# Kernel optimization log

Hardware: AMD Instinct MI355X
Metric: run time of the kernel (lower is better)

## Reference

```python
import jax, jax.numpy as jnp
import numpy as np

CONF_THRESH = 0.3
NMS_THRESH = 0.5
TOP_K = 64
VAR = (0.1, 0.2)  # standard SSD decode variances


def setup_inputs() -> dict:
    key = jax.random.key(0)
    k1, k2, k3 = jax.random.split(key, 3)
    B, A, C = 16, 16384, 81
    loc = jax.random.normal(k1, (B, A, 4), jnp.float32)
    conf = jax.random.normal(k2, (B, A, C), jnp.float32)
    anchors = jax.random.uniform(k3, (A, 4), jnp.float32)  # cxcywh in [0,1]
    return {"loc": loc, "conf": conf, "anchors": anchors}


def _decode(loc, anchors):
    # SSD-style decode: loc [A,4] offsets, anchors [A,4] cxcywh -> corners [A,4]
    cxcy = anchors[:, :2] + loc[:, :2] * VAR[0] * anchors[:, 2:]
    wh = anchors[:, 2:] * jnp.exp(loc[:, 2:] * VAR[1])
    tl = cxcy - wh * 0.5
    return jnp.concatenate([tl, tl + wh], axis=1)


def _iou(box, boxes):
    # box [4], boxes [A,4] in corner format
    tl = jnp.maximum(box[:2], boxes[:, :2])
    br = jnp.minimum(box[2:], boxes[:, 2:])
    wh = jnp.clip(br - tl, 0.0)
    inter = wh[:, 0] * wh[:, 1]
    a1 = (box[2] - box[0]) * (box[3] - box[1])
    a2 = (boxes[:, 2] - boxes[:, 0]) * (boxes[:, 3] - boxes[:, 1])
    return inter / (a1 + a2 - inter)


def _nms(boxes, scores):
    # greedy NMS for one (batch, class) lane; boxes [A,4], scores [A]
    s0 = jnp.where(scores > CONF_THRESH, scores, -1.0)

    def step(s, _):
        i = jnp.argmax(s)
        sc = s[i]
        box = boxes[i]
        keep = sc > 0.0  # -1 means masked/suppressed; valid scores > conf_thresh > 0
        supp = jnp.where(_iou(box, boxes) > NMS_THRESH, -1.0, s).at[i].set(-1.0)
        s_next = jnp.where(keep, supp, s)
        row = jnp.where(keep, jnp.concatenate([sc[None], box]),
                        jnp.zeros((5,), s.dtype))
        return s_next, row

    _, rows = jax.lax.scan(step, s0, None, length=TOP_K)
    return rows  # [TOP_K, 5] = (score, x1, y1, x2, y2), zero-padded


def reference(loc, conf, anchors):
    conf = jax.nn.sigmoid(conf)                      # [B,A,C]
    boxes = jax.vmap(_decode, in_axes=(0, None))(loc, anchors)  # [B,A,4]
    scores = jnp.swapaxes(conf, 1, 2)                # [B,C,A]
    per_class = jax.vmap(_nms, in_axes=(None, 0))    # over classes
    out = jax.vmap(per_class)(boxes, scores)         # [B,C,TOP_K,5]
    return out
```

## Files before the change

### kernel.cpp

```cpp
#include <hip/hip_runtime.h>
#include <math.h>

constexpr int B_N  = 16;
constexpr int A_N  = 16384;
constexpr int C_N  = 81;
constexpr int TOPK = 64;
constexpr int DNT  = 256;
constexpr int NBINS = 232;
constexpr int CAP   = 512;
constexpr unsigned BIN_BASE = 0x3E99u;

constexpr int TA   = 64;
constexpr int TPAD = 85;
constexpr int TNT  = 256;
constexpr int TILE_ELEMS = TA * C_N;
constexpr int TILE_F4    = (TA / 4) * C_N;

constexpr int SNT = 256;

__global__ __launch_bounds__(DNT) void decode_kernel(const float4* __restrict__ loc,
                                                     const float4* __restrict__ anch,
                                                     float4* __restrict__ boxes) {
    int i = blockIdx.x * DNT + threadIdx.x;
    int a = i & (A_N - 1);
    float4 l  = loc[i];
    float4 an = anch[a];
    float cx = an.x + (l.x * 0.1f) * an.z;
    float cy = an.y + (l.y * 0.1f) * an.w;
    float w  = an.z * expf(l.z * 0.2f);
    float h  = an.w * expf(l.w * 0.2f);
    float x1 = cx - w * 0.5f;
    float y1 = cy - h * 0.5f;
    boxes[i] = make_float4(x1, y1, x1 + w, y1 + h);
}

__global__ __launch_bounds__(TNT) void sigT_kernel(const float* __restrict__ conf,
                                                   float* __restrict__ scoresT) {
    __shared__ float tile[TA][TPAD];

    const int a0 = blockIdx.x * TA;
    const int b  = blockIdx.y;
    const int t  = threadIdx.x;

    const float* src = conf + ((size_t)b * A_N + a0) * C_N;
#pragma unroll
    for (int i = 0; i < (TILE_ELEMS + TNT - 1) / TNT; ++i) {
        int idx = i * TNT + t;
        if (idx < TILE_ELEMS) {
            float x  = src[idx];
            int   al = idx / C_N;
            int   cc = idx - al * C_N;
            tile[al][cc] = 1.0f / (1.0f + expf(-x));
        }
    }
    __syncthreads();
    float* dst = scoresT + (size_t)b * C_N * A_N + a0;
#pragma unroll
    for (int i = 0; i < (TILE_F4 + TNT - 1) / TNT; ++i) {
        int idx4 = i * TNT + t;
        if (idx4 < TILE_F4) {
            int cc  = idx4 >> 4;
            int al4 = idx4 & 15;
            float4 v;
            v.x = tile[al4 * 4 + 0][cc];
            v.y = tile[al4 * 4 + 1][cc];
            v.z = tile[al4 * 4 + 2][cc];
            v.w = tile[al4 * 4 + 3][cc];
            ((float4*)(dst + (size_t)cc * A_N))[al4] = v;
        }
    }
}

__global__ __launch_bounds__(SNT, 4) void select_nms_kernel(
        const float* __restrict__ scoresT,
        const float4* __restrict__ boxes,
        float* __restrict__ out) {
    __shared__ int hist[NBINS];
    __shared__ unsigned long long cand[CAP];
    __shared__ float4 cbox[CAP];
    __shared__ int s_cnt, s_acc, s_kout;

    const int bc   = blockIdx.x;
    const int b    = bc / C_N;
    const int t    = threadIdx.x;
    const int lane = t & 63;
    const int wv   = t >> 6;

    for (int i = t; i < NBINS; i += SNT) hist[i] = 0;
    if (t == 0) { s_acc = 0; s_kout = 0; }
    __syncthreads();

    const float4* sptr = (const float4*)(scoresT + (size_t)bc * A_N);
    const float4* bptr = boxes + (size_t)b * A_N;
    float* optr = out + (size_t)bc * TOPK * 5;

    for (int i = 0; i < A_N / 4 / SNT; ++i) {
        float4 s4 = sptr[t + SNT * i];
        float s[4] = {s4.x, s4.y, s4.z, s4.w};
#pragma unroll
        for (int q = 0; q < 4; ++q) {
            if (s[q] > 0.3f) {
                unsigned u = __float_as_uint(s[q]);
                int bin = (int)(u >> 16) - (int)BIN_BASE;
                bin = bin < 0 ? 0 : (bin > NBINS - 1 ? NBINS - 1 : bin);
                atomicAdd(&hist[bin], 1);
            }
        }
    }
    __syncthreads();

    float rx1 = 0.f, ry1 = 0.f, rx2 = 0.f, ry2 = 0.f, rar = 0.f;
    int acc = 0, kout = 0;

    int bin_hi = NBINS;
    for (;;) {
        int lo = bin_hi, tot = 0;
        while (lo > 0) {
            int cnt = hist[lo - 1];
            if (tot + cnt > CAP) {
                if (tot == 0) { lo--; }
                break;
            }
            tot += cnt; lo--;
        }
        const int bin_lo = lo;
        if (bin_lo == bin_hi) break;
        if (t == 0) s_cnt = 0;
        __syncthreads();

        for (int i = 0; i < A_N / 4 / SNT; ++i) {
            float4 s4 = sptr[t + SNT * i];
            float s[4] = {s4.x, s4.y, s4.z, s4.w};
#pragma unroll
            for (int q = 0; q < 4; ++q) {
                if (s[q] > 0.3f) {
                    unsigned u = __float_as_uint(s[q]);
                    int bin = (int)(u >> 16) - (int)BIN_BASE;
                    bin = bin < 0 ? 0 : (bin > NBINS - 1 ? NBINS - 1 : bin);
                    if (bin >= bin_lo && bin < bin_hi) {
                        int slot = atomicAdd(&s_cnt, 1);
                        if (slot < CAP) {
                            unsigned a = (unsigned)(4 * (t + SNT * i) + q);
                            cand[slot] = ((unsigned long long)u << 32) | (unsigned)(~a);
                        }
                    }
                }
            }
        }
        __syncthreads();
        int C = s_cnt; if (C > CAP) C = CAP;

        if (C > 0) {
            if (wv == 0) {
                unsigned long long key[8];
#pragma unroll
                for (int r = 0; r < 8; ++r) {
                    int sidx = r * 64 + lane;
                    key[r] = (sidx < C) ? cand[sidx] : 0ull;
                }
#pragma unroll
                for (int k = 2; k <= CAP; k <<= 1) {
#pragma unroll
                    for (int j = k >> 1; j > 0; j >>= 1) {
                        if (j >= 64) {
                            int jr = j >> 6;
#pragma unroll
                            for (int r = 0; r < 8; ++r) {
                                int rp = r ^ jr;
                                if (rp > r) {
                                    int e = r * 64 + lane;
                                    bool up = ((e & k) == 0);
                                    unsigned long long va = key[r], vb = key[rp];
                                    bool sw = up ? (va < vb) : (va > vb);
                                    if (sw) { key[r] = vb; key[rp] = va; }
                                }
                            }
                        } else {
#pragma unroll
                            for (int r = 0; r < 8; ++r) {
                                int e = r * 64 + lane;
                                bool up    = ((e & k) == 0);
                                bool isLow = ((lane & j) == 0);
                                unsigned long long va = key[r];
                                unsigned long long vb = __shfl_xor(va, j, 64);
                                bool keepMax = (up == isLow);
                                key[r] = keepMax ? (va > vb ? va : vb)
                                                 : (va < vb ? va : vb);
                            }
                        }
                    }
                }
#pragma unroll
                for (int r = 0; r < 8; ++r) cand[r * 64 + lane] = key[r];
            }
            __syncthreads();

            for (int e = t; e < CAP; e += SNT)
                if (e < C) cbox[e] = bptr[(int)(~(unsigned)cand[e])];
            __syncthreads();

            if (wv == 0) {
                int ts = 0;
                unsigned long long k0 = cand[0];
                float4 cb = cbox[0];
                while (ts < C) {
                    unsigned long long nk = 0ull;
                    float4 nb = cb;
                    if (ts + 1 < C) { nk = cand[ts + 1]; nb = cbox[ts + 1]; }
                    float sc = __uint_as_float((unsigned)(k0 >> 32));
                    float ca = (cb.z - cb.x) * (cb.w - cb.y);
                    bool over = false;
                    if (lane < acc) {
                        float tlx = fmaxf(rx1, cb.x);
                        float tly = fmaxf(ry1, cb.y);
                        float brx = fminf(rx2, cb.z);
                        float bry = fminf(ry2, cb.w);
                        float iw  = fmaxf(brx - tlx, 0.0f);
                        float ih  = fmaxf(bry - tly, 0.0f);
                        float inter = iw * ih;
                        float iou = inter / (rar + ca - inter);
                        over = iou > 0.5f;
                    }
                    if (!__any(over)) {
                        if (lane == acc) { rx1 = cb.x; ry1 = cb.y; rx2 = cb.z; ry2 = cb.w; rar = ca; }
                        if (lane == 0) {
                            float* o = optr + (size_t)kout * 5;
                            o[0] = sc; o[1] = cb.x; o[2] = cb.y; o[3] = cb.z; o[4] = cb.w;
                        }
                        acc++; kout++;
                        if (acc == TOPK) break;
                    }
                    ++ts; k0 = nk; cb = nb;
                }
                if (lane == 0) { s_acc = acc; s_kout = kout; }
            }
            __syncthreads();
            if (s_acc >= TOPK) break;
        }
        bin_hi = bin_lo;
    }

    {
        const int ko = s_kout;
        float* o  = optr + (size_t)ko * 5;
        int   rem = (TOPK - ko) * 5;
        for (int i = t; i < rem; i += SNT) o[i] = 0.0f;
    }
}

__device__ __forceinline__ void sort_gather_scan64(
        unsigned long long* cand, float4* cbox, int C, int lane,
        const float4* __restrict__ bptr, float* __restrict__ optr,
        float& rx1, float& ry1, float& rx2, float& ry2, float& rar,
        int& acc, int& kout) {
    unsigned long long key[8];
#pragma unroll
    for (int r = 0; r < 8; ++r) {
        int sidx = r * 64 + lane;
        key[r] = (sidx < C) ? cand[sidx] : 0ull;
    }
#pragma unroll
    for (int k = 2; k <= CAP; k <<= 1) {
#pragma unroll
        for (int j = k >> 1; j > 0; j >>= 1) {
            if (j >= 64) {
                int jr = j >> 6;
#pragma unroll
                for (int r = 0; r < 8; ++r) {
                    int rp = r ^ jr;
                    if (rp > r) {
                        int e = r * 64 + lane;
                        bool up = ((e & k) == 0);
                        unsigned long long va = key[r], vb = key[rp];
                        bool sw = up ? (va < vb) : (va > vb);
                        if (sw) { key[r] = vb; key[rp] = va; }
                    }
                }
            } else {
#pragma unroll
                for (int r = 0; r < 8; ++r) {
                    int e = r * 64 + lane;
                    bool up    = ((e & k) == 0);
                    bool isLow = ((lane & j) == 0);
                    unsigned long long va = key[r];
                    unsigned long long vb = __shfl_xor(va, j, 64);
                    bool keepMax = (up == isLow);
                    key[r] = keepMax ? (va > vb ? va : vb) : (va < vb ? va : vb);
                }
            }
        }
    }
    __syncthreads();
#pragma unroll
    for (int r = 0; r < 8; ++r) cand[r * 64 + lane] = key[r];
    __syncthreads();
#pragma unroll
    for (int r = 0; r < 8; ++r) {
        int e = r * 64 + lane;
        if (e < C) cbox[e] = bptr[(int)(~(unsigned)cand[e])];
    }
    __syncthreads();

    int t = 0;
    unsigned long long k0 = cand[0];
    float4 cb = cbox[0];
    while (t < C) {
        unsigned long long nk = 0ull;
        float4 nb = cb;
        if (t + 1 < C) { nk = cand[t + 1]; nb = cbox[t + 1]; }
        float sc = __uint_as_float((unsigned)(k0 >> 32));
        float ca = (cb.z - cb.x) * (cb.w - cb.y);
        bool over = false;
        if (lane < acc) {
            float tlx = fmaxf(rx1, cb.x);
            float tly = fmaxf(ry1, cb.y);
            float brx = fminf(rx2, cb.z);
            float bry = fminf(ry2, cb.w);
            float iw  = fmaxf(brx - tlx, 0.0f);
            float ih  = fmaxf(bry - tly, 0.0f);
            float inter = iw * ih;
            float iou = inter / (rar + ca - inter);
            over = iou > 0.5f;
        }
        if (!__any(over)) {
            if (lane == acc) { rx1 = cb.x; ry1 = cb.y; rx2 = cb.z; ry2 = cb.w; rar = ca; }
            if (lane == 0) {
                float* o = optr + (size_t)kout * 5;
                o[0] = sc; o[1] = cb.x; o[2] = cb.y; o[3] = cb.z; o[4] = cb.w;
            }
            acc++; kout++;
            if (acc == TOPK) break;
        }
        ++t; k0 = nk; cb = nb;
    }
}

__global__ __launch_bounds__(64, 4) void nms_fallback(const float* __restrict__ conf,
                                                      const float4* __restrict__ boxes,
                                                      float* __restrict__ out) {
    __shared__ int hist[NBINS];
    __shared__ unsigned long long cand[CAP];
    __shared__ float4 cbox[CAP];
    __shared__ int s_cnt;

    const int c    = blockIdx.x;
    const int b    = blockIdx.y;
    const int lane = threadIdx.x;

    const float4* bptr = boxes + (size_t)b * A_N;
    const float*  cptr = conf + (size_t)b * A_N * C_N + c;
    float* optr = out + (size_t)(b * C_N + c) * TOPK * 5;

    for (int i = lane; i < NBINS; i += 64) hist[i] = 0;
    __syncthreads();
    for (int i = 0; i < A_N / 256; ++i) {
        int a0 = 4 * (lane + 64 * i);
#pragma unroll
        for (int q = 0; q < 4; ++q) {
            float x = cptr[(size_t)(a0 + q) * C_N];
            float s = 1.0f / (1.0f + expf(-x));
            if (s > 0.3f) {
                unsigned u = __float_as_uint(s);
                int bin = (int)(u >> 16) - (int)BIN_BASE;
                bin = bin < 0 ? 0 : (bin > NBINS - 1 ? NBINS - 1 : bin);
                atomicAdd(&hist[bin], 1);
            }
        }
    }
    __syncthreads();

    float rx1 = 0.f, ry1 = 0.f, rx2 = 0.f, ry2 = 0.f, rar = 0.f;
    int acc = 0, kout = 0;
    int bin_hi = NBINS;
    for (;;) {
        int lo = bin_hi, tot = 0;
        while (lo > 0) {
            int cnt = hist[lo - 1];
            if (tot + cnt > CAP) { if (tot == 0) { lo--; } break; }
            tot += cnt; lo--;
        }
        const int bin_lo = lo;
        if (bin_lo == bin_hi) break;
        if (lane == 0) s_cnt = 0;
        __syncthreads();
        for (int i = 0; i < A_N / 256; ++i) {
            int a0 = 4 * (lane + 64 * i);
#pragma unroll
            for (int q = 0; q < 4; ++q) {
                float x = cptr[(size_t)(a0 + q) * C_N];
                float s = 1.0f / (1.0f + expf(-x));
                if (s > 0.3f) {
                    unsigned u = __float_as_uint(s);
                    int bin = (int)(u >> 16) - (int)BIN_BASE;
                    bin = bin < 0 ? 0 : (bin > NBINS - 1 ? NBINS - 1 : bin);
                    if (bin >= bin_lo && bin < bin_hi) {
                        int slot = atomicAdd(&s_cnt, 1);
                        if (slot < CAP)
                            cand[slot] = ((unsigned long long)u << 32) | (unsigned)(~(unsigned)(a0 + q));
                    }
                }
            }
        }
        __syncthreads();
        int C = s_cnt; if (C > CAP) C = CAP;
        if (C > 0)
            sort_gather_scan64(cand, cbox, C, lane, bptr, optr,
                               rx1, ry1, rx2, ry2, rar, acc, kout);
        if (acc == TOPK) break;
        bin_hi = bin_lo;
    }
    {
        float* o  = optr + (size_t)kout * 5;
        int   rem = (TOPK - kout) * 5;
        for (int i = lane; i < rem; i += 64) o[i] = 0.0f;
    }
}

extern "C" void kernel_launch(void* const* d_in, const int* in_sizes, int n_in,
                              void* d_out, int out_size, void* d_ws, size_t ws_size,
                              hipStream_t stream) {
    const float* loc     = (const float*)d_in[0];
    const float* conf    = (const float*)d_in[1];
    const float* anchors = (const float*)d_in[2];
    float* out = (float*)d_out;

    const size_t boxes_bytes  = (size_t)B_N * A_N * sizeof(float4);
    const size_t scores_bytes = (size_t)B_N * C_N * A_N * sizeof(float);

    float4* boxes = (float4*)d_ws;

    decode_kernel<<<(B_N * A_N) / DNT, DNT, 0, stream>>>(
        (const float4*)loc, (const float4*)anchors, boxes);

    if (ws_size >= boxes_bytes + scores_bytes) {
        float* scoresT = (float*)((char*)d_ws + boxes_bytes);
        sigT_kernel<<<dim3(A_N / TA, B_N), TNT, 0, stream>>>(conf, scoresT);
        select_nms_kernel<<<dim3(B_N * C_N), SNT, 0, stream>>>(scoresT, boxes, out);
    } else {
        nms_fallback<<<dim3(C_N, B_N), 64, 0, stream>>>(conf, boxes, out);
    }
}
```

Measured before the change: 220.6 us.

## Use single-wave select-NMS blocks and vectorized float4 sigmoid loads in transpose

The select/NMS kernel now runs with one 64-thread wave per (batch,class) instead of 256 threads, reusing the existing wave-level sort/gather/scan helper. This removes the block-wide barriers and the idle waves during the sort and scan phases, but each wave now scans all 16384 scores by itself. The sigmoid-transpose kernel also loads conf as float4 into an unpadded flat shared tile, where the old version used scalar loads. This may add shared-memory bank conflicts on the strided transposed reads.

```diff
diff --git a/kernel.cpp b/kernel.cpp
--- a/kernel.cpp
+++ b/kernel.cpp
@@ -11,12 +11,9 @@
 constexpr unsigned BIN_BASE = 0x3E99u;
 
 constexpr int TA   = 64;
-constexpr int TPAD = 85;
 constexpr int TNT  = 256;
 constexpr int TILE_ELEMS = TA * C_N;
-constexpr int TILE_F4    = (TA / 4) * C_N;
-
-constexpr int SNT = 256;
+constexpr int TILE_F4    = TILE_ELEMS / 4;
 
 __global__ __launch_bounds__(DNT) void decode_kernel(const float4* __restrict__ loc,
                                                      const float4* __restrict__ anch,
@@ -36,21 +33,25 @@
 
 __global__ __launch_bounds__(TNT) void sigT_kernel(const float* __restrict__ conf,
                                                    float* __restrict__ scoresT) {
-    __shared__ float tile[TA][TPAD];
+    __shared__ float4 tile4[TILE_F4];
+    float* tile = (float*)tile4;
 
     const int a0 = blockIdx.x * TA;
     const int b  = blockIdx.y;
     const int t  = threadIdx.x;
 
-    const float* src = conf + ((size_t)b * A_N + a0) * C_N;
-#pragma unroll
-    for (int i = 0; i < (TILE_ELEMS + TNT - 1) / TNT; ++i) {
-        int idx = i * TNT + t;
-        if (idx < TILE_ELEMS) {
-            float x  = src[idx];
-            int   al = idx / C_N;
-            int   cc = idx - al * C_N;
-            tile[al][cc] = 1.0f / (1.0f + expf(-x));
+    const float4* src = (const float4*)(conf + ((size_t)b * A_N + a0) * C_N);
+#pragma unroll
+    for (int i = 0; i < (TILE_F4 + TNT - 1) / TNT; ++i) {
+        int idx4 = i * TNT + t;
+        if (idx4 < TILE_F4) {
+            float4 x = src[idx4];
+            float4 v;
+            v.x = 1.0f / (1.0f + expf(-x.x));
+            v.y = 1.0f / (1.0f + expf(-x.y));
+            v.z = 1.0f / (1.0f + expf(-x.z));
+            v.w = 1.0f / (1.0f + expf(-x.w));
+            tile4[idx4] = v;
         }
     }
     __syncthreads();
@@ -61,190 +62,14 @@
         if (idx4 < TILE_F4) {
             int cc  = idx4 >> 4;
             int al4 = idx4 & 15;
+            int e   = al4 * 4 * C_N + cc;
             float4 v;
-            v.x = tile[al4 * 4 + 0][cc];
-            v.y = tile[al4 * 4 + 1][cc];
-            v.z = tile[al4 * 4 + 2][cc];
-            v.w = tile[al4 * 4 + 3][cc];
+            v.x = tile[e];
+            v.y = tile[e + C_N];
+            v.z = tile[e + 2 * C_N];
+            v.w = tile[e + 3 * C_N];
             ((float4*)(dst + (size_t)cc * A_N))[al4] = v;
         }
-    }
-}
-
-__global__ __launch_bounds__(SNT, 4) void select_nms_kernel(
-        const float* __restrict__ scoresT,
-        const float4* __restrict__ boxes,
-        float* __restrict__ out) {
-    __shared__ int hist[NBINS];
-    __shared__ unsigned long long cand[CAP];
-    __shared__ float4 cbox[CAP];
-    __shared__ int s_cnt, s_acc, s_kout;
-
-    const int bc   = blockIdx.x;
-    const int b    = bc / C_N;
-    const int t    = threadIdx.x;
-    const int lane = t & 63;
-    const int wv   = t >> 6;
-
-    for (int i = t; i < NBINS; i += SNT) hist[i] = 0;
-    if (t == 0) { s_acc = 0; s_kout = 0; }
-    __syncthreads();
-
-    const float4* sptr = (const float4*)(scoresT + (size_t)bc * A_N);
-    const float4* bptr = boxes + (size_t)b * A_N;
-    float* optr = out + (size_t)bc * TOPK * 5;
-
-    for (int i = 0; i < A_N / 4 / SNT; ++i) {
-        float4 s4 = sptr[t + SNT * i];
-        float s[4] = {s4.x, s4.y, s4.z, s4.w};
-#pragma unroll
-        for (int q = 0; q < 4; ++q) {
-            if (s[q] > 0.3f) {
-                unsigned u = __float_as_uint(s[q]);
-                int bin = (int)(u >> 16) - (int)BIN_BASE;
-                bin = bin < 0 ? 0 : (bin > NBINS - 1 ? NBINS - 1 : bin);
-                atomicAdd(&hist[bin], 1);
-            }
-        }
-    }
-    __syncthreads();
-
-    float rx1 = 0.f, ry1 = 0.f, rx2 = 0.f, ry2 = 0.f, rar = 0.f;
-    int acc = 0, kout = 0;
-
-    int bin_hi = NBINS;
-    for (;;) {
-        int lo = bin_hi, tot = 0;
-        while (lo > 0) {
-            int cnt = hist[lo - 1];
-            if (tot + cnt > CAP) {
-                if (tot == 0) { lo--; }
-                break;
-            }
-            tot += cnt; lo--;
-        }
-        const int bin_lo = lo;
-        if (bin_lo == bin_hi) break;
-        if (t == 0) s_cnt = 0;
-        __syncthreads();
-
-        for (int i = 0; i < A_N / 4 / SNT; ++i) {
-            float4 s4 = sptr[t + SNT * i];
-            float s[4] = {s4.x, s4.y, s4.z, s4.w};
-#pragma unroll
-            for (int q = 0; q < 4; ++q) {
-                if (s[q] > 0.3f) {
-                    unsigned u = __float_as_uint(s[q]);
-                    int bin = (int)(u >> 16) - (int)BIN_BASE;
-                    bin = bin < 0 ? 0 : (bin > NBINS - 1 ? NBINS - 1 : bin);
-                    if (bin >= bin_lo && bin < bin_hi) {
-                        int slot = atomicAdd(&s_cnt, 1);
-                        if (slot < CAP) {
-                            unsigned a = (unsigned)(4 * (t + SNT * i) + q);
-                            cand[slot] = ((unsigned long long)u << 32) | (unsigned)(~a);
-                        }
-                    }
-                }
-            }
-        }
-        __syncthreads();
-        int C = s_cnt; if (C > CAP) C = CAP;
-
-        if (C > 0) {
-            if (wv == 0) {
-                unsigned long long key[8];
-#pragma unroll
-                for (int r = 0; r < 8; ++r) {
-                    int sidx = r * 64 + lane;
-                    key[r] = (sidx < C) ? cand[sidx] : 0ull;
-                }
-#pragma unroll
-                for (int k = 2; k <= CAP; k <<= 1) {
-#pragma unroll
-                    for (int j = k >> 1; j > 0; j >>= 1) {
-                        if (j >= 64) {
-                            int jr = j >> 6;
-#pragma unroll
-                            for (int r = 0; r < 8; ++r) {
-                                int rp = r ^ jr;
-                                if (rp > r) {
-                                    int e = r * 64 + lane;
-                                    bool up = ((e & k) == 0);
-                                    unsigned long long va = key[r], vb = key[rp];
-                                    bool sw = up ? (va < vb) : (va > vb);
-                                    if (sw) { key[r] = vb; key[rp] = va; }
-                                }
-                            }
-                        } else {
-#pragma unroll
-                            for (int r = 0; r < 8; ++r) {
-                                int e = r * 64 + lane;
-                                bool up    = ((e & k) == 0);
-                                bool isLow = ((lane & j) == 0);
-                                unsigned long long va = key[r];
-                                unsigned long long vb = __shfl_xor(va, j, 64);
-                                bool keepMax = (up == isLow);
-                                key[r] = keepMax ? (va > vb ? va : vb)
-                                                 : (va < vb ? va : vb);
-                            }
-                        }
-                    }
-                }
-#pragma unroll
-                for (int r = 0; r < 8; ++r) cand[r * 64 + lane] = key[r];
-            }
-            __syncthreads();
-
-            for (int e = t; e < CAP; e += SNT)
-                if (e < C) cbox[e] = bptr[(int)(~(unsigned)cand[e])];
-            __syncthreads();
-
-            if (wv == 0) {
-                int ts = 0;
-                unsigned long long k0 = cand[0];
-                float4 cb = cbox[0];
-                while (ts < C) {
-                    unsigned long long nk = 0ull;
-                    float4 nb = cb;
-                    if (ts + 1 < C) { nk = cand[ts + 1]; nb = cbox[ts + 1]; }
-                    float sc = __uint_as_float((unsigned)(k0 >> 32));
-                    float ca = (cb.z - cb.x) * (cb.w - cb.y);
-                    bool over = false;
-                    if (lane < acc) {
-                        float tlx = fmaxf(rx1, cb.x);
-                        float tly = fmaxf(ry1, cb.y);
-                        float brx = fminf(rx2, cb.z);
-                        float bry = fminf(ry2, cb.w);
-                        float iw  = fmaxf(brx - tlx, 0.0f);
-                        float ih  = fmaxf(bry - tly, 0.0f);
-                        float inter = iw * ih;
-                        float iou = inter / (rar + ca - inter);
-                        over = iou > 0.5f;
-                    }
-                    if (!__any(over)) {
-                        if (lane == acc) { rx1 = cb.x; ry1 = cb.y; rx2 = cb.z; ry2 = cb.w; rar = ca; }
-                        if (lane == 0) {
-                            float* o = optr + (size_t)kout * 5;
-                            o[0] = sc; o[1] = cb.x; o[2] = cb.y; o[3] = cb.z; o[4] = cb.w;
-                        }
-                        acc++; kout++;
-                        if (acc == TOPK) break;
-                    }
-                    ++ts; k0 = nk; cb = nb;
-                }
-                if (lane == 0) { s_acc = acc; s_kout = kout; }
-            }
-            __syncthreads();
-            if (s_acc >= TOPK) break;
-        }
-        bin_hi = bin_lo;
-    }
-
-    {
-        const int ko = s_kout;
-        float* o  = optr + (size_t)ko * 5;
-        int   rem = (TOPK - ko) * 5;
-        for (int i = t; i < rem; i += SNT) o[i] = 0.0f;
     }
 }
 
@@ -301,13 +126,13 @@
     }
     __syncthreads();
 
-    int t = 0;
+    int ts = 0;
     unsigned long long k0 = cand[0];
     float4 cb = cbox[0];
-    while (t < C) {
+    while (ts < C) {
         unsigned long long nk = 0ull;
         float4 nb = cb;
-        if (t + 1 < C) { nk = cand[t + 1]; nb = cbox[t + 1]; }
+        if (ts + 1 < C) { nk = cand[ts + 1]; nb = cbox[ts + 1]; }
         float sc = __uint_as_float((unsigned)(k0 >> 32));
         float ca = (cb.z - cb.x) * (cb.w - cb.y);
         bool over = false;
@@ -331,7 +156,99 @@
             acc++; kout++;
             if (acc == TOPK) break;
         }
-        ++t; k0 = nk; cb = nb;
+        ++ts; k0 = nk; cb = nb;
+    }
+}
+
+__global__ __launch_bounds__(64, 4) void select_nms_kernel(
+        const float* __restrict__ scoresT,
+        const float4* __restrict__ boxes,
+        float* __restrict__ out) {
+    __shared__ int hist[NBINS];
+    __shared__ unsigned long long cand[CAP];
+    __shared__ float4 cbox[CAP];
+    __shared__ int s_cnt;
+
+    const int bc   = blockIdx.x;
+    const int b    = bc / C_N;
+    const int lane = threadIdx.x;
+
+    for (int i = lane; i < NBINS; i += 64) hist[i] = 0;
+    __syncthreads();
+
+    const float4* sptr = (const float4*)(scoresT + (size_t)bc * A_N);
+    const float4* bptr = boxes + (size_t)b * A_N;
+    float* optr = out + (size_t)bc * TOPK * 5;
+
+#pragma unroll 8
+    for (int i = 0; i < A_N / 4 / 64; ++i) {
+        float4 s4 = sptr[lane + 64 * i];
+        float s[4] = {s4.x, s4.y, s4.z, s4.w};
+#pragma unroll
+        for (int q = 0; q < 4; ++q) {
+            if (s[q] > 0.3f) {
+                unsigned u = __float_as_uint(s[q]);
+                int bin = (int)(u >> 16) - (int)BIN_BASE;
+                bin = bin < 0 ? 0 : (bin > NBINS - 1 ? NBINS - 1 : bin);
+                atomicAdd(&hist[bin], 1);
+            }
+        }
+    }
+    __syncthreads();
+
+    float rx1 = 0.f, ry1 = 0.f, rx2 = 0.f, ry2 = 0.f, rar = 0.f;
+    int acc = 0, kout = 0;
+
+    int bin_hi = NBINS;
+    for (;;) {
+        int lo = bin_hi, tot = 0;
+        while (lo > 0) {
+            int cnt = hist[lo - 1];
+            if (tot + cnt > CAP) {
+                if (tot == 0) { lo--; }
+                break;
+            }
+            tot += cnt; lo--;
+        }
+        const int bin_lo = lo;
+        if (bin_lo == bin_hi) break;
+        if (lane == 0) s_cnt = 0;
+        __syncthreads();
+
+#pragma unroll 8
+        for (int i = 0; i < A_N / 4 / 64; ++i) {
+            float4 s4 = sptr[lane + 64 * i];
+            float s[4] = {s4.x, s4.y, s4.z, s4.w};
+#pragma unroll
+            for (int q = 0; q < 4; ++q) {
+                if (s[q] > 0.3f) {
+                    unsigned u = __float_as_uint(s[q]);
+                    int bin = (int)(u >> 16) - (int)BIN_BASE;
+                    bin = bin < 0 ? 0 : (bin > NBINS - 1 ? NBINS - 1 : bin);
+                    if (bin >= bin_lo && bin < bin_hi) {
+                        int slot = atomicAdd(&s_cnt, 1);
+                        if (slot < CAP) {
+                            unsigned a = (unsigned)(4 * (lane + 64 * i) + q);
+                            cand[slot] = ((unsigned long long)u << 32) | (unsigned)(~a);
+                        }
+                    }
+                }
+            }
+        }
+        __syncthreads();
+        int C = s_cnt; if (C > CAP) C = CAP;
+
+        if (C > 0)
+            sort_gather_scan64(cand, cbox, C, lane, bptr, optr,
+                               rx1, ry1, rx2, ry2, rar, acc, kout);
+        if (acc == TOPK) break;
+        bin_hi = bin_lo;
+    }
+
+    {
+        float* o  = optr + (size_t)kout * 5;
+        int   rem = (TOPK - kout) * 5;
+        for (int i = lane; i < rem; i += 64) o[i] = 0.0f;
     }
 }
 
@@ -435,7 +352,7 @@
     if (ws_size >= boxes_bytes + scores_bytes) {
         float* scoresT = (float*)((char*)d_ws + boxes_bytes);
         sigT_kernel<<<dim3(A_N / TA, B_N), TNT, 0, stream>>>(conf, scoresT);
-        select_nms_kernel<<<dim3(B_N * C_N), SNT, 0, stream>>>(scoresT, boxes, out);
+        select_nms_kernel<<<dim3(B_N * C_N), 64, 0, stream>>>(scoresT, boxes, out);
     } else {
         nms_fallback<<<dim3(C_N, B_N), 64, 0, stream>>>(conf, boxes, out);
     }
```

New measurement: 258.7 us. +17.3%, slower.

## Split select+NMS into histogram/candidate kernel and single-wave sorted NMS kernel

Applied to the files above, without the earlier changes.

The fused select+NMS kernel is split in two. A 256-thread select kernel builds the score histogram and writes the top-bin candidates to global workspace. A separate 64-thread NMS kernel then sorts those candidates and runs the serial greedy scan, rescanning scores only when it needs more candidates. Separately, the sigmoid/transpose kernel now loads conf with float4 vectorized reads into an unpadded shared tile. The split stops the serial NMS phase from idling three waves per block, at the cost of an extra launch, global round trips for candidates and histograms, and possible LDS bank conflicts from removing the padding.

```diff
diff --git a/kernel.cpp b/kernel.cpp
--- a/kernel.cpp
+++ b/kernel.cpp
@@ -9,14 +9,13 @@
 constexpr int NBINS = 232;
 constexpr int CAP   = 512;
 constexpr unsigned BIN_BASE = 0x3E99u;
+constexpr int SNT = 256;
+constexpr int BC_N = B_N * C_N;
 
 constexpr int TA   = 64;
-constexpr int TPAD = 85;
 constexpr int TNT  = 256;
 constexpr int TILE_ELEMS = TA * C_N;
-constexpr int TILE_F4    = (TA / 4) * C_N;
-
-constexpr int SNT = 256;
+constexpr int TILE_F4    = TILE_ELEMS / 4;
 
 __global__ __launch_bounds__(DNT) void decode_kernel(const float4* __restrict__ loc,
                                                      const float4* __restrict__ anch,
@@ -36,21 +35,25 @@
 
 __global__ __launch_bounds__(TNT) void sigT_kernel(const float* __restrict__ conf,
                                                    float* __restrict__ scoresT) {
-    __shared__ float tile[TA][TPAD];
+    __shared__ float4 tile4[TILE_F4];
+    float* tile = (float*)tile4;
 
     const int a0 = blockIdx.x * TA;
     const int b  = blockIdx.y;
     const int t  = threadIdx.x;
 
-    const float* src = conf + ((size_t)b * A_N + a0) * C_N;
-#pragma unroll
-    for (int i = 0; i < (TILE_ELEMS + TNT - 1) / TNT; ++i) {
-        int idx = i * TNT + t;
-        if (idx < TILE_ELEMS) {
-            float x  = src[idx];
-            int   al = idx / C_N;
-            int   cc = idx - al * C_N;
-            tile[al][cc] = 1.0f / (1.0f + expf(-x));
+    const float4* src = (const float4*)(conf + ((size_t)b * A_N + a0) * C_N);
+#pragma unroll
+    for (int i = 0; i < (TILE_F4 + TNT - 1) / TNT; ++i) {
+        int idx4 = i * TNT + t;
+        if (idx4 < TILE_F4) {
+            float4 x = src[idx4];
+            float4 v;
+            v.x = 1.0f / (1.0f + expf(-x.x));
+            v.y = 1.0f / (1.0f + expf(-x.y));
+            v.z = 1.0f / (1.0f + expf(-x.z));
+            v.w = 1.0f / (1.0f + expf(-x.w));
+            tile4[idx4] = v;
         }
     }
     __syncthreads();
@@ -61,17 +64,264 @@
         if (idx4 < TILE_F4) {
             int cc  = idx4 >> 4;
             int al4 = idx4 & 15;
+            int e   = al4 * 4 * C_N + cc;
             float4 v;
-            v.x = tile[al4 * 4 + 0][cc];
-            v.y = tile[al4 * 4 + 1][cc];
-            v.z = tile[al4 * 4 + 2][cc];
-            v.w = tile[al4 * 4 + 3][cc];
+            v.x = tile[e];
+            v.y = tile[e + C_N];
+            v.z = tile[e + 2 * C_N];
+            v.w = tile[e + 3 * C_N];
             ((float4*)(dst + (size_t)cc * A_N))[al4] = v;
         }
     }
 }
 
-__global__ __launch_bounds__(SNT, 4) void select_nms_kernel(
+__device__ __forceinline__ void sort_gather_scan64(
+        unsigned long long* cand, float4* cbox, int C, int lane,
+        const float4* __restrict__ bptr, float* __restrict__ optr,
+        float& rx1, float& ry1, float& rx2, float& ry2, float& rar,
+        int& acc, int& kout) {
+    unsigned long long key[8];
+#pragma unroll
+    for (int r = 0; r < 8; ++r) {
+        int sidx = r * 64 + lane;
+        key[r] = (sidx < C) ? cand[sidx] : 0ull;
+    }
+#pragma unroll
+    for (int k = 2; k <= CAP; k <<= 1) {
+#pragma unroll
+        for (int j = k >> 1; j > 0; j >>= 1) {
+            if (j >= 64) {
+                int jr = j >> 6;
+#pragma unroll
+                for (int r = 0; r < 8; ++r) {
+                    int rp = r ^ jr;
+                    if (rp > r) {
+                        int e = r * 64 + lane;
+                        bool up = ((e & k) == 0);
+                        unsigned long long va = key[r], vb = key[rp];
+                        bool sw = up ? (va < vb) : (va > vb);
+                        if (sw) { key[r] = vb; key[rp] = va; }
+                    }
+                }
+            } else {
+#pragma unroll
+                for (int r = 0; r < 8; ++r) {
+                    int e = r * 64 + lane;
+                    bool up    = ((e & k) == 0);
+                    bool isLow = ((lane & j) == 0);
+                    unsigned long long va = key[r];
+                    unsigned long long vb = __shfl_xor(va, j, 64);
+                    bool keepMax = (up == isLow);
+                    key[r] = keepMax ? (va > vb ? va : vb) : (va < vb ? va : vb);
+                }
+            }
+        }
+    }
+    __syncthreads();
+#pragma unroll
+    for (int r = 0; r < 8; ++r) cand[r * 64 + lane] = key[r];
+    __syncthreads();
+#pragma unroll
+    for (int r = 0; r < 8; ++r) {
+        int e = r * 64 + lane;
+        if (e < C) cbox[e] = bptr[(int)(~(unsigned)cand[e])];
+    }
+    __syncthreads();
+
+    int ts = 0;
+    unsigned long long k0 = cand[0];
+    float4 cb = cbox[0];
+    while (ts < C) {
+        unsigned long long nk = 0ull;
+        float4 nb = cb;
+        if (ts + 1 < C) { nk = cand[ts + 1]; nb = cbox[ts + 1]; }
+        float sc = __uint_as_float((unsigned)(k0 >> 32));
+        float ca = (cb.z - cb.x) * (cb.w - cb.y);
+        bool over = false;
+        if (lane < acc) {
+            float tlx = fmaxf(rx1, cb.x);
+            float tly = fmaxf(ry1, cb.y);
+            float brx = fminf(rx2, cb.z);
+            float bry = fminf(ry2, cb.w);
+            float iw  = fmaxf(brx - tlx, 0.0f);
+            float ih  = fmaxf(bry - tly, 0.0f);
+            float inter = iw * ih;
+            float iou = inter / (rar + ca - inter);
+            over = iou > 0.5f;
+        }
+        if (!__any(over)) {
+            if (lane == acc) { rx1 = cb.x; ry1 = cb.y; rx2 = cb.z; ry2 = cb.w; rar = ca; }
+            if (lane == 0) {
+                float* o = optr + (size_t)kout * 5;
+                o[0] = sc; o[1] = cb.x; o[2] = cb.y; o[3] = cb.z; o[4] = cb.w;
+            }
+            acc++; kout++;
+            if (acc == TOPK) break;
+        }
+        ++ts; k0 = nk; cb = nb;
+    }
+}
+
+__global__ __launch_bounds__(SNT) void select_kernel(
+        const float* __restrict__ scoresT,
+        unsigned long long* __restrict__ g_cand,
+        int* __restrict__ g_hist,
+        int* __restrict__ g_cnt,
+        int* __restrict__ g_blo) {
+    __shared__ int hist[NBINS];
+    __shared__ int s_cnt;
+
+    const int bc = blockIdx.x;
+    const int t  = threadIdx.x;
+
+    for (int i = t; i < NBINS; i += SNT) hist[i] = 0;
+    if (t == 0) s_cnt = 0;
+    __syncthreads();
+
+    const float4* sptr = (const float4*)(scoresT + (size_t)bc * A_N);
+
+    for (int i = 0; i < A_N / 4 / SNT; ++i) {
+        float4 s4 = sptr[t + SNT * i];
+        float s[4] = {s4.x, s4.y, s4.z, s4.w};
+#pragma unroll
+        for (int q = 0; q < 4; ++q) {
+            if (s[q] > 0.3f) {
+                unsigned u = __float_as_uint(s[q]);
+                int bin = (int)(u >> 16) - (int)BIN_BASE;
+                bin = bin < 0 ? 0 : (bin > NBINS - 1 ? NBINS - 1 : bin);
+                atomicAdd(&hist[bin], 1);
+            }
+        }
+    }
+    __syncthreads();
+
+    for (int i = t; i < NBINS; i += SNT) g_hist[bc * NBINS + i] = hist[i];
+
+    int lo = NBINS, tot = 0;
+    while (lo > 0) {
+        int cnt = hist[lo - 1];
+        if (tot + cnt > CAP) {
+            if (tot == 0) { lo--; }
+            break;
+        }
+        tot += cnt; lo--;
+    }
+    const int bin_lo = lo;
+
+    if (bin_lo < NBINS) {
+        for (int i = 0; i < A_N / 4 / SNT; ++i) {
+            float4 s4 = sptr[t + SNT * i];
+            float s[4] = {s4.x, s4.y, s4.z, s4.w};
+#pragma unroll
+            for (int q = 0; q < 4; ++q) {
+                if (s[q] > 0.3f) {
+                    unsigned u = __float_as_uint(s[q]);
+                    int bin = (int)(u >> 16) - (int)BIN_BASE;
+                    bin = bin < 0 ? 0 : (bin > NBINS - 1 ? NBINS - 1 : bin);
+                    if (bin >= bin_lo && bin < NBINS) {
+                        int slot = atomicAdd(&s_cnt, 1);
+                        if (slot < CAP) {
+                            unsigned a = (unsigned)(4 * (t + SNT * i) + q);
+                            g_cand[(size_t)bc * CAP + slot] =
+                                ((unsigned long long)u << 32) | (unsigned)(~a);
+                        }
+                    }
+                }
+            }
+        }
+    }
+    __syncthreads();
+    if (t == 0) {
+        int C = s_cnt; if (C > CAP) C = CAP;
+        g_cnt[bc] = C;
+        g_blo[bc] = bin_lo;
+    }
+}
+
+__global__ __launch_bounds__(64, 4) void nms_sorted_kernel(
+        const float* __restrict__ scoresT,
+        const float4* __restrict__ boxes,
+        const unsigned long long* __restrict__ g_cand,
+        const int* __restrict__ g_hist,
+        const int* __restrict__ g_cnt,
+        const int* __restrict__ g_blo,
+        float* __restrict__ out) {
+    __shared__ int hist[NBINS];
+    __shared__ unsigned long long cand[CAP];
+    __shared__ float4 cbox[CAP];
+    __shared__ int s_cnt;
+
+    const int bc   = blockIdx.x;
+    const int b    = bc / C_N;
+    const int lane = threadIdx.x;
+
+    const float4* sptr = (const float4*)(scoresT + (size_t)bc * A_N);
+    const float4* bptr = boxes + (size_t)b * A_N;
+    float* optr = out + (size_t)bc * TOPK * 5;
+
+    for (int i = lane; i < NBINS; i += 64) hist[i] = g_hist[bc * NBINS + i];
+    const int C0 = g_cnt[bc];
+    int bin_hi   = g_blo[bc];
+    for (int e = lane; e < C0; e += 64) cand[e] = g_cand[(size_t)bc * CAP + e];
+    __syncthreads();
+
+    float rx1 = 0.f, ry1 = 0.f, rx2 = 0.f, ry2 = 0.f, rar = 0.f;
+    int acc = 0, kout = 0;
+
+    if (C0 > 0)
+        sort_gather_scan64(cand, cbox, C0, lane, bptr, optr,
+                           rx1, ry1, rx2, ry2, rar, acc, kout);
+
+    while (acc < TOPK) {
+        int lo = bin_hi, tot = 0;
+        while (lo > 0) {
+            int cnt = hist[lo - 1];
+            if (tot + cnt > CAP) {
+                if (tot == 0) { lo--; }
+                break;
+            }
+            tot += cnt; lo--;
+        }
+        const int bin_lo = lo;
+        if (bin_lo == bin_hi) break;
+        if (lane == 0) s_cnt = 0;
+        __syncthreads();
+
+        for (int i = 0; i < A_N / 4 / 64; ++i) {
+            float4 s4 = sptr[lane + 64 * i];
+            float s[4] = {s4.x, s4.y, s4.z, s4.w};
+#pragma unroll
+            for (int q = 0; q < 4; ++q) {
+                if (s[q] > 0.3f) {
+                    unsigned u = __float_as_uint(s[q]);
+                    int bin = (int)(u >> 16) - (int)BIN_BASE;
+                    bin = bin < 0 ? 0 : (bin > NBINS - 1 ? NBINS - 1 : bin);
+                    if (bin >= bin_lo && bin < bin_hi) {
+                        int slot = atomicAdd(&s_cnt, 1);
+                        if (slot < CAP) {
+                            unsigned a = (unsigned)(4 * (lane + 64 * i) + q);
+                            cand[slot] = ((unsigned long long)u << 32) | (unsigned)(~a);
+                        }
+                    }
+                }
+            }
+        }
+        __syncthreads();
+        int C = s_cnt; if (C > CAP) C = CAP;
+        if (C > 0)
+            sort_gather_scan64(cand, cbox, C, lane, bptr, optr,
+                               rx1, ry1, rx2, ry2, rar, acc, kout);
+        bin_hi = bin_lo;
+    }
+
+    {
+        float* o  = optr + (size_t)kout * 5;
+        int   rem = (TOPK - kout) * 5;
+        for (int i = lane; i < rem; i += 64) o[i] = 0.0f;
+    }
+}
+
+__global__ __launch_bounds__(SNT, 4) void select_nms_fused(
         const float* __restrict__ scoresT,
         const float4* __restrict__ boxes,
         float* __restrict__ out) {
@@ -117,10 +367,7 @@
         int lo = bin_hi, tot = 0;
         while (lo > 0) {
             int cnt = hist[lo - 1];
-            if (tot + cnt > CAP) {
-                if (tot == 0) { lo--; }
-                break;
-            }
+            if (tot + cnt > CAP) { if (tot == 0) { lo--; } break; }
             tot += cnt; lo--;
         }
         const int bin_lo = lo;
@@ -248,93 +495,6 @@
     }
 }
 
-__device__ __forceinline__ void sort_gather_scan64(
-        unsigned long long* cand, float4* cbox, int C, int lane,
-        const float4* __restrict__ bptr, float* __restrict__ optr,
-        float& rx1, float& ry1, float& rx2, float& ry2, float& rar,
-        int& acc, int& kout) {
-    unsigned long long key[8];
-#pragma unroll
-    for (int r = 0; r < 8; ++r) {
-        int sidx = r * 64 + lane;
-        key[r] = (sidx < C) ? cand[sidx] : 0ull;
-    }
-#pragma unroll
-    for (int k = 2; k <= CAP; k <<= 1) {
-#pragma unroll
-        for (int j = k >> 1; j > 0; j >>= 1) {
-            if (j >= 64) {
-                int jr = j >> 6;
-#pragma unroll
-                for (int r = 0; r < 8; ++r) {
-                    int rp = r ^ jr;
-                    if (rp > r) {
-                        int e = r * 64 + lane;
-                        bool up = ((e & k) == 0);
-                        unsigned long long va = key[r], vb = key[rp];
-                        bool sw = up ? (va < vb) : (va > vb);
-                        if (sw) { key[r] = vb; key[rp] = va; }
-                    }
-                }
-            } else {
-#pragma unroll
-                for (int r = 0; r < 8; ++r) {
-                    int e = r * 64 + lane;
-                    bool up    = ((e & k) == 0);
-                    bool isLow = ((lane & j) == 0);
-                    unsigned long long va = key[r];
-                    unsigned long long vb = __shfl_xor(va, j, 64);
-                    bool keepMax = (up == isLow);
-                    key[r] = keepMax ? (va > vb ? va : vb) : (va < vb ? va : vb);
-                }
-            }
-        }
-    }
-    __syncthreads();
-#pragma unroll
-    for (int r = 0; r < 8; ++r) cand[r * 64 + lane] = key[r];
-    __syncthreads();
-#pragma unroll
-    for (int r = 0; r < 8; ++r) {
-        int e = r * 64 + lane;
-        if (e < C) cbox[e] = bptr[(int)(~(unsigned)cand[e])];
-    }
-    __syncthreads();
-
-    int t = 0;
-    unsigned long long k0 = cand[0];
-    float4 cb = cbox[0];
-    while (t < C) {
-        unsigned long long nk = 0ull;
-        float4 nb = cb;
-        if (t + 1 < C) { nk = cand[t + 1]; nb = cbox[t + 1]; }
-        float sc = __uint_as_float((unsigned)(k0 >> 32));
-        float ca = (cb.z - cb.x) * (cb.w - cb.y);
-        bool over = false;
-        if (lane < acc) {
-            float tlx = fmaxf(rx1, cb.x);
-            float tly = fmaxf(ry1, cb.y);
-            float brx = fminf(rx2, cb.z);
-            float bry = fminf(ry2, cb.w);
-            float iw  = fmaxf(brx - tlx, 0.0f);
-            float ih  = fmaxf(bry - tly, 0.0f);
-            float inter = iw * ih;
-            float iou = inter / (rar + ca - inter);
-            over = iou > 0.5f;
-        }
-        if (!__any(over)) {
-            if (lane == acc) { rx1 = cb.x; ry1 = cb.y; rx2 = cb.z; ry2 = cb.w; rar = ca; }
-            if (lane == 0) {
-                float* o = optr + (size_t)kout * 5;
-                o[0] = sc; o[1] = cb.x; o[2] = cb.y; o[3] = cb.z; o[4] = cb.w;
-            }
-            acc++; kout++;
-            if (acc == TOPK) break;
-        }
-        ++t; k0 = nk; cb = nb;
-    }
-}
-
 __global__ __launch_bounds__(64, 4) void nms_fallback(const float* __restrict__ conf,
                                                       const float4* __restrict__ boxes,
                                                       float* __restrict__ out) {
@@ -426,16 +586,33 @@
 
     const size_t boxes_bytes  = (size_t)B_N * A_N * sizeof(float4);
     const size_t scores_bytes = (size_t)B_N * C_N * A_N * sizeof(float);
+    const size_t cand_bytes   = (size_t)BC_N * CAP * sizeof(unsigned long long);
+    const size_t hist_bytes   = (size_t)BC_N * NBINS * sizeof(int);
+    const size_t cnt_bytes    = (size_t)BC_N * sizeof(int);
+    const size_t full_bytes   = boxes_bytes + scores_bytes + cand_bytes +
+                                hist_bytes + 2 * cnt_bytes;
 
     float4* boxes = (float4*)d_ws;
 
     decode_kernel<<<(B_N * A_N) / DNT, DNT, 0, stream>>>(
         (const float4*)loc, (const float4*)anchors, boxes);
 
-    if (ws_size >= boxes_bytes + scores_bytes) {
+    if (ws_size >= full_bytes) {
+        char* p = (char*)d_ws + boxes_bytes;
+        float* scoresT = (float*)p;                 p += scores_bytes;
+        unsigned long long* g_cand = (unsigned long long*)p; p += cand_bytes;
+        int* g_hist = (int*)p;                      p += hist_bytes;
+        int* g_cnt  = (int*)p;                      p += cnt_bytes;
+        int* g_blo  = (int*)p;
+
+        sigT_kernel<<<dim3(A_N / TA, B_N), TNT, 0, stream>>>(conf, scoresT);
+        select_kernel<<<dim3(BC_N), SNT, 0, stream>>>(scoresT, g_cand, g_hist, g_cnt, g_blo);
+        nms_sorted_kernel<<<dim3(BC_N), 64, 0, stream>>>(scoresT, boxes, g_cand,
+                                                         g_hist, g_cnt, g_blo, out);
+    } else if (ws_size >= boxes_bytes + scores_bytes) {
         float* scoresT = (float*)((char*)d_ws + boxes_bytes);
         sigT_kernel<<<dim3(A_N / TA, B_N), TNT, 0, stream>>>(conf, scoresT);
-        select_nms_kernel<<<dim3(B_N * C_N), SNT, 0, stream>>>(scoresT, boxes, out);
+        select_nms_fused<<<dim3(BC_N), SNT, 0, stream>>>(scoresT, boxes, out);
     } else {
         nms_fallback<<<dim3(C_N, B_N), 64, 0, stream>>>(conf, boxes, out);
     }
```

After: 221.7 us. No clear change (+0.5%).

## Process NMS candidates in pairs and vectorize sigmoid transpose tile loads

Applied to the files above, without the earlier changes.

The greedy NMS scan now tests two candidates per iteration against the kept boxes, plus a direct pairwise check between them, which halves the serial wave-vote steps. The IoU > 0.5 test is rewritten without a division, as a double-precision comparison against a constant just above one half, meant to give the same decisions as the reference. The sigmoid-transpose kernel now loads conf as float4 into an unpadded shared tile, which cuts global load instructions but may add LDS bank conflicts on the strided reads in the transpose phase. The double-precision compare and the extra per-iteration work cost something on every pair.

```diff
diff --git a/kernel.cpp b/kernel.cpp
--- a/kernel.cpp
+++ b/kernel.cpp
@@ -9,14 +9,14 @@
 constexpr int NBINS = 232;
 constexpr int CAP   = 512;
 constexpr unsigned BIN_BASE = 0x3E99u;
+constexpr int SNT = 256;
+
+#define IOU_HALF_EXACT 0x1.000001p-1
 
 constexpr int TA   = 64;
-constexpr int TPAD = 85;
 constexpr int TNT  = 256;
 constexpr int TILE_ELEMS = TA * C_N;
-constexpr int TILE_F4    = (TA / 4) * C_N;
-
-constexpr int SNT = 256;
+constexpr int TILE_F4    = TILE_ELEMS / 4;
 
 __global__ __launch_bounds__(DNT) void decode_kernel(const float4* __restrict__ loc,
                                                      const float4* __restrict__ anch,
@@ -36,21 +36,25 @@
 
 __global__ __launch_bounds__(TNT) void sigT_kernel(const float* __restrict__ conf,
                                                    float* __restrict__ scoresT) {
-    __shared__ float tile[TA][TPAD];
+    __shared__ float4 tile4[TILE_F4];
+    float* tile = (float*)tile4;
 
     const int a0 = blockIdx.x * TA;
     const int b  = blockIdx.y;
     const int t  = threadIdx.x;
 
-    const float* src = conf + ((size_t)b * A_N + a0) * C_N;
-#pragma unroll
-    for (int i = 0; i < (TILE_ELEMS + TNT - 1) / TNT; ++i) {
-        int idx = i * TNT + t;
-        if (idx < TILE_ELEMS) {
-            float x  = src[idx];
-            int   al = idx / C_N;
-            int   cc = idx - al * C_N;
-            tile[al][cc] = 1.0f / (1.0f + expf(-x));
+    const float4* src = (const float4*)(conf + ((size_t)b * A_N + a0) * C_N);
+#pragma unroll
+    for (int i = 0; i < (TILE_F4 + TNT - 1) / TNT; ++i) {
+        int idx4 = i * TNT + t;
+        if (idx4 < TILE_F4) {
+            float4 x = src[idx4];
+            float4 v;
+            v.x = 1.0f / (1.0f + expf(-x.x));
+            v.y = 1.0f / (1.0f + expf(-x.y));
+            v.z = 1.0f / (1.0f + expf(-x.z));
+            v.w = 1.0f / (1.0f + expf(-x.w));
+            tile4[idx4] = v;
         }
     }
     __syncthreads();
@@ -61,14 +65,29 @@
         if (idx4 < TILE_F4) {
             int cc  = idx4 >> 4;
             int al4 = idx4 & 15;
+            int e   = al4 * 4 * C_N + cc;
             float4 v;
-            v.x = tile[al4 * 4 + 0][cc];
-            v.y = tile[al4 * 4 + 1][cc];
-            v.z = tile[al4 * 4 + 2][cc];
-            v.w = tile[al4 * 4 + 3][cc];
+            v.x = tile[e];
+            v.y = tile[e + C_N];
+            v.z = tile[e + 2 * C_N];
+            v.w = tile[e + 3 * C_N];
             ((float4*)(dst + (size_t)cc * A_N))[al4] = v;
         }
     }
+}
+
+__device__ __forceinline__ bool iou_gt_half(float Ax1, float Ay1, float Ax2,
+                                            float Ay2, float aA,
+                                            const float4& Bx, float aB) {
+    float tlx = fmaxf(Ax1, Bx.x);
+    float tly = fmaxf(Ay1, Bx.y);
+    float brx = fminf(Ax2, Bx.z);
+    float bry = fminf(Ay2, Bx.w);
+    float iw  = fmaxf(brx - tlx, 0.0f);
+    float ih  = fmaxf(bry - tly, 0.0f);
+    float inter = iw * ih;
+    float den = aA + aB - inter;
+    return (double)inter > (double)den * IOU_HALF_EXACT;
 }
 
 __global__ __launch_bounds__(SNT, 4) void select_nms_kernel(
@@ -201,41 +220,53 @@
 
             if (wv == 0) {
                 int ts = 0;
-                unsigned long long k0 = cand[0];
-                float4 cb = cbox[0];
                 while (ts < C) {
-                    unsigned long long nk = 0ull;
-                    float4 nb = cb;
-                    if (ts + 1 < C) { nk = cand[ts + 1]; nb = cbox[ts + 1]; }
-                    float sc = __uint_as_float((unsigned)(k0 >> 32));
-                    float ca = (cb.z - cb.x) * (cb.w - cb.y);
-                    bool over = false;
+                    unsigned long long k0 = cand[ts];
+                    float4 cb = cbox[ts];
+                    const bool have1 = (ts + 1 < C);
+                    unsigned long long k1 = have1 ? cand[ts + 1] : 0ull;
+                    float4 b1 = have1 ? cbox[ts + 1] : cb;
+                    float ca0 = (cb.z - cb.x) * (cb.w - cb.y);
+                    float ca1 = (b1.z - b1.x) * (b1.w - b1.y);
+
+                    bool over0 = false, over1 = false;
                     if (lane < acc) {
-                        float tlx = fmaxf(rx1, cb.x);
-                        float tly = fmaxf(ry1, cb.y);
-                        float brx = fminf(rx2, cb.z);
-                        float bry = fminf(ry2, cb.w);
-                        float iw  = fmaxf(brx - tlx, 0.0f);
-                        float ih  = fmaxf(bry - tly, 0.0f);
-                        float inter = iw * ih;
-                        float iou = inter / (rar + ca - inter);
-                        over = iou > 0.5f;
-                    }
-                    if (!__any(over)) {
-                        if (lane == acc) { rx1 = cb.x; ry1 = cb.y; rx2 = cb.z; ry2 = cb.w; rar = ca; }
+                        over0 = iou_gt_half(rx1, ry1, rx2, ry2, rar, cb, ca0);
+                        over1 = iou_gt_half(rx1, ry1, rx2, ry2, rar, b1, ca1);
+                    }
+                    bool kill01 = have1 &&
+                        iou_gt_half(cb.x, cb.y, cb.z, cb.w, ca0, b1, ca1);
+
+                    bool acc0 = !__any(over0);
+                    bool any1 = __any(over1);
+
+                    if (acc0) {
+                        if (lane == acc) { rx1 = cb.x; ry1 = cb.y; rx2 = cb.z; ry2 = cb.w; rar = ca0; }
                         if (lane == 0) {
                             float* o = optr + (size_t)kout * 5;
-                            o[0] = sc; o[1] = cb.x; o[2] = cb.y; o[3] = cb.z; o[4] = cb.w;
+                            o[0] = __uint_as_float((unsigned)(k0 >> 32));
+                            o[1] = cb.x; o[2] = cb.y; o[3] = cb.z; o[4] = cb.w;
                         }
                         acc++; kout++;
                         if (acc == TOPK) break;
                     }
-                    ++ts; k0 = nk; cb = nb;
+                    if (have1 && !any1 && !(acc0 && kill01)) {
+                        if (lane == acc) { rx1 = b1.x; ry1 = b1.y; rx2 = b1.z; ry2 = b1.w; rar = ca1; }
+                        if (lane == 0) {
+                            float* o = optr + (size_t)kout * 5;
+                            o[0] = __uint_as_float((unsigned)(k1 >> 32));
+                            o[1] = b1.x; o[2] = b1.y; o[3] = b1.z; o[4] = b1.w;
+                        }
+                        acc++; kout++;
+                        if (acc == TOPK) break;
+                    }
+                    ts += 2;
                 }
                 if (lane == 0) { s_acc = acc; s_kout = kout; }
             }
             __syncthreads();
             if (s_acc >= TOPK) break;
+            if (wv == 0) acc = s_acc;
         }
         bin_hi = bin_lo;
     }
```

Result: faster. 216.1 us (-2.0%).
